# Kernel tuning notes

Hardware: AMD Instinct MI355X
Metric: run time of the kernel (lower is better)

## Reference

```python
import jax, jax.numpy as jnp
import numpy as np

M, K, N = 65536, 512, 512
EPS = 1e-05


def setup_inputs() -> dict:
    key = jax.random.key(0)
    k1, k2, k3 = jax.random.split(key, 3)
    x = jax.random.normal(k1, (M, K), dtype=jnp.float32)
    # int8 weight buffer in [-128, 127]
    weight_int8 = jax.random.randint(k2, (N, K), -128, 128, dtype=jnp.int32).astype(jnp.int8)
    # realistic per-output-channel dequant scales (max-abs / 127 of an fp weight)
    weight_scale = jax.random.uniform(k3, (N,), dtype=jnp.float32, minval=0.001, maxval=0.02)
    return {"x": x, "weight_int8": weight_int8, "weight_scale": weight_scale}


def reference(x, weight_int8, weight_scale):
    # dynamic per-tensor quantization of the activation
    x_scale = jnp.maximum(jnp.max(jnp.abs(x)) / 127.0, EPS)
    x_int8 = jnp.clip(jnp.round(x / x_scale), -128, 127).astype(jnp.int8)
    out_int32 = jnp.matmul(x_int8, weight_int8.T, preferred_element_type=jnp.int32)
    # dequantize: per-tensor input scale * per-row weight scale
    out = out_int32.astype(jnp.float32) * (x_scale * weight_scale[None, :])
    return out
```

## Files before the change

### kernel.cpp

```cpp
#include <hip/hip_runtime.h>


#define M_DIM 65536
#define K_DIM 512
#define N_DIM 512
#define EPSF  1e-5f

typedef int int32x4 __attribute__((ext_vector_type(4)));

#define WS_PART   256
#define WS_WPACK  32768

__device__ inline unsigned int pack_w4(int4 v) {
    return (v.x & 0xff) | ((v.y & 0xff) << 8) |
           ((v.z & 0xff) << 16) | ((unsigned)v.w << 24);
}

__device__ inline unsigned int quantpack4(float4 f, float inv) {
    const float C = 12582912.0f;
    unsigned int u0 = __float_as_uint(fmaf(f.x, inv, C));
    unsigned int u1 = __float_as_uint(fmaf(f.y, inv, C));
    unsigned int u2 = __float_as_uint(fmaf(f.z, inv, C));
    unsigned int u3 = __float_as_uint(fmaf(f.w, inv, C));
    unsigned int lo = __builtin_amdgcn_perm(u1, u0, 0x0C0C0400u);
    unsigned int hi = __builtin_amdgcn_perm(u3, u2, 0x04000C0Cu);
    return lo | hi;
}

__global__ void absmax1_pack_kernel(const float* __restrict__ x,
                                    const int* __restrict__ wi,
                                    float* __restrict__ partials,
                                    unsigned int* __restrict__ wp) {
    const int b = blockIdx.x;
    const int t = threadIdx.x;
    if (b < 4096) {
        __shared__ float red[4];
        const float4* x4 = (const float4*)x;
        const int base = b * 2048;
        float m = 0.0f;
        #pragma unroll
        for (int j = 0; j < 8; ++j) {
            float4 v = x4[base + j * 256 + t];
            m = fmaxf(m, fmaxf(fmaxf(fabsf(v.x), fabsf(v.y)),
                               fmaxf(fabsf(v.z), fabsf(v.w))));
        }
        #pragma unroll
        for (int off = 32; off > 0; off >>= 1)
            m = fmaxf(m, __shfl_xor(m, off));
        if ((t & 63) == 0) red[t >> 6] = m;
        __syncthreads();
        if (t == 0)
            partials[b] = fmaxf(fmaxf(red[0], red[1]), fmaxf(red[2], red[3]));
    } else {
        const int bb = b - 4096;
        #pragma unroll
        for (int j = 0; j < 4; ++j) {
            int d = bb * 1024 + j * 256 + t;
            wp[d] = pack_w4(((const int4*)wi)[d]);
        }
    }
}

__global__ __launch_bounds__(256, 2) void fused_quant_gemm_kernel(
    const float* __restrict__ x, const signed char* __restrict__ w,
    const float* __restrict__ wscale, const float* __restrict__ partials,
    float* __restrict__ out) {
    __shared__ __attribute__((aligned(16))) signed char Lds[64 * 1024];
    __shared__ float red[4];

    const int t    = threadIdx.x;
    const int wave = t >> 6;
    const int lane = t & 63;
    const int quad = lane >> 4;
    const int l16  = lane & 15;
    const int m0   = blockIdx.x * 128;

    float m = 0.0f;
    {
        const float4* p4 = (const float4*)partials;
        #pragma unroll
        for (int j = 0; j < 4; ++j) {
            float4 v = p4[t + j * 256];
            m = fmaxf(m, fmaxf(fmaxf(v.x, v.y), fmaxf(v.z, v.w)));
        }
        #pragma unroll
        for (int off = 32; off > 0; off >>= 1)
            m = fmaxf(m, __shfl_xor(m, off));
        if (lane == 0) red[wave] = m;
    }
    __syncthreads();
    const float mx  = fmaxf(fmaxf(red[0], red[1]), fmaxf(red[2], red[3]));
    const float s   = fmaxf(mx / 127.0f, EPSF);
    const float inv = 1.0f / s;
    __syncthreads();

    {
        const float4* xs = (const float4*)(x + (size_t)m0 * K_DIM);
        const int rsub = t >> 5;
        const int csub = (t & 31) * 16;
        #pragma unroll
        for (int j = 0; j < 16; ++j) {
            const int fi = j * 1024 + t * 4;
            float4 v0 = xs[fi + 0];
            float4 v1 = xs[fi + 1];
            float4 v2 = xs[fi + 2];
            float4 v3 = xs[fi + 3];
            int32x4 p;
            p.x = (int)quantpack4(v0, inv);
            p.y = (int)quantpack4(v1, inv);
            p.z = (int)quantpack4(v2, inv);
            p.w = (int)quantpack4(v3, inv);
            const int row  = j * 8 + rsub;
            const int addr = (row * 512 + csub) ^ ((row & 7) << 4);
            *(int32x4*)(Lds + addr) = p;
        }
    }
    __syncthreads();

    int32x4 a0[8], a1[8];
    {
        const int r0 = wave * 32 + l16;
        const int r1 = r0 + 16;
        #pragma unroll
        for (int k = 0; k < 8; ++k) {
            const int c = quad * 16 + k * 64;
            a0[k] = *(const int32x4*)(Lds + ((r0 * 512 + c) ^ ((r0 & 7) << 4)));
            a1[k] = *(const int32x4*)(Lds + ((r1 * 512 + c) ^ ((r1 & 7) << 4)));
        }
    }
    __syncthreads();

    const int mw = m0 + wave * 32;

    for (int bx = 0; bx < 4; ++bx) {
        const int n0 = bx * 128;

        #pragma unroll
        for (int cc = 0; cc < 2; ++cc) {
            int c = wave * 2 + cc;
            #pragma unroll
            for (int tt = 0; tt < 8; ++tt) {
                const signed char* g = w + (long)(n0 + tt * 16 + l16) * K_DIM
                                         + c * 64 + quad * 16;
                __builtin_amdgcn_global_load_lds(
                    (const __attribute__((address_space(1))) unsigned int*)g,
                    (__attribute__((address_space(3))) unsigned int*)(Lds + (c * 8 + tt) * 1024),
                    16, 0, 0);
            }
        }
        __syncthreads();

        int32x4 acc0[8] = {};
        int32x4 acc1[8] = {};
        #pragma unroll
        for (int k = 0; k < 8; ++k) {
            const signed char* bbase = Lds + k * 8192 + lane * 16;
            #pragma unroll
            for (int tt = 0; tt < 8; ++tt) {
                int32x4 b = *(const int32x4*)(bbase + tt * 1024);
                acc0[tt] = __builtin_amdgcn_mfma_i32_16x16x64_i8(a0[k], b, acc0[tt], 0, 0, 0);
                acc1[tt] = __builtin_amdgcn_mfma_i32_16x16x64_i8(a1[k], b, acc1[tt], 0, 0, 0);
            }
        }

        #pragma unroll
        for (int tt = 0; tt < 8; ++tt) {
            int n = n0 + tt * 16 + l16;
            float c = s * wscale[n];
            float* o0 = out + (long)(mw + quad * 4) * N_DIM + n;
            float* o1 = o0 + (long)16 * N_DIM;
            #pragma unroll
            for (int r = 0; r < 4; ++r) {
                o0[(long)r * N_DIM] = (float)acc0[tt][r] * c;
                o1[(long)r * N_DIM] = (float)acc1[tt][r] * c;
            }
        }
        if (bx < 3) __syncthreads();
    }
}

extern "C" void kernel_launch(void* const* d_in, const int* in_sizes, int n_in,
                              void* d_out, int out_size, void* d_ws, size_t ws_size,
                              hipStream_t stream) {
    const float* x   = (const float*)d_in[0];
    const int*   wi  = (const int*)d_in[1];
    const float* sc  = (const float*)d_in[2];
    float*       out = (float*)d_out;

    float*        partials = (float*)((char*)d_ws + WS_PART);
    unsigned int* wp       = (unsigned int*)((char*)d_ws + WS_WPACK);
    const signed char* w8  = (const signed char*)wp;

    absmax1_pack_kernel<<<4160, 256, 0, stream>>>(x, wi, partials, wp);
    fused_quant_gemm_kernel<<<512, 256, 0, stream>>>(x, w8, sc, partials, out);
}
```

Measured before the change: 265.7 us.

## Fuse absmax and GEMM into one persistent kernel with grid-wide atomic barrier

Merges the absmax/weight-pack kernel into the GEMM kernel. Each block computes its own tile's absmax while holding half of its activations in registers, then joins a grid-wide barrier built on an atomic counter before quantizing directly into MFMA A fragments, which skips the LDS staging round trip. The weight tile load for the next N-block is now issued before the current block's output stores, so the fetch overlaps the epilogue. The barrier relies on all 512 blocks being co-resident, and the large register array (h[32] plus the fragments) raises register pressure, which risks spills or deadlock if occupancy assumptions fail.

After: 381.2 us. 43.5% more time.

```diff
diff --git a/kernel.cpp b/kernel.cpp
--- a/kernel.cpp
+++ b/kernel.cpp
@@ -5,9 +5,11 @@
 #define K_DIM 512
 #define N_DIM 512
 #define EPSF  1e-5f
+#define GRID  512
 
 typedef int int32x4 __attribute__((ext_vector_type(4)));
 
+#define WS_CNT    0
 #define WS_PART   256
 #define WS_WPACK  32768
 
@@ -27,139 +29,162 @@
     return lo | hi;
 }
 
-__global__ void absmax1_pack_kernel(const float* __restrict__ x,
-                                    const int* __restrict__ wi,
-                                    float* __restrict__ partials,
-                                    unsigned int* __restrict__ wp) {
-    const int b = blockIdx.x;
-    const int t = threadIdx.x;
-    if (b < 4096) {
-        __shared__ float red[4];
-        const float4* x4 = (const float4*)x;
-        const int base = b * 2048;
-        float m = 0.0f;
-        #pragma unroll
-        for (int j = 0; j < 8; ++j) {
-            float4 v = x4[base + j * 256 + t];
-            m = fmaxf(m, fmaxf(fmaxf(fabsf(v.x), fabsf(v.y)),
-                               fmaxf(fabsf(v.z), fabsf(v.w))));
-        }
-        #pragma unroll
-        for (int off = 32; off > 0; off >>= 1)
-            m = fmaxf(m, __shfl_xor(m, off));
-        if ((t & 63) == 0) red[t >> 6] = m;
-        __syncthreads();
-        if (t == 0)
-            partials[b] = fmaxf(fmaxf(red[0], red[1]), fmaxf(red[2], red[3]));
-    } else {
-        const int bb = b - 4096;
-        #pragma unroll
-        for (int j = 0; j < 4; ++j) {
-            int d = bb * 1024 + j * 256 + t;
-            wp[d] = pack_w4(((const int4*)wi)[d]);
-        }
-    }
-}
-
-__global__ __launch_bounds__(256, 2) void fused_quant_gemm_kernel(
-    const float* __restrict__ x, const signed char* __restrict__ w,
-    const float* __restrict__ wscale, const float* __restrict__ partials,
+__global__ __launch_bounds__(256, 2) void fused_kernel(
+    const float* __restrict__ x, const int* __restrict__ wi,
+    const float* __restrict__ wscale, unsigned int* __restrict__ ws,
     float* __restrict__ out) {
-    __shared__ __attribute__((aligned(16))) signed char Lds[64 * 1024];
+    __shared__ __attribute__((aligned(16))) signed char Blds[64 * 1024];
     __shared__ float red[4];
+
+    unsigned int* cnt      = ws + (WS_CNT >> 2);
+    unsigned int* partials = ws + (WS_PART >> 2);
+    unsigned int* wp       = ws + (WS_WPACK >> 2);
+    const signed char* w8  = (const signed char*)wp;
 
     const int t    = threadIdx.x;
     const int wave = t >> 6;
     const int lane = t & 63;
     const int quad = lane >> 4;
     const int l16  = lane & 15;
-    const int m0   = blockIdx.x * 128;
-
+    const int b    = blockIdx.x;
+    const int m0   = b * 128;
+    const int mw   = m0 + wave * 32;
+
+    const float* xr0 = x + (size_t)(mw + l16) * K_DIM + quad * 16;
+    const float* xr1 = xr0 + (size_t)16 * K_DIM;
+
+    float4 h[32];
     float m = 0.0f;
+    #pragma unroll
+    for (int k = 0; k < 8; ++k) {
+        #pragma unroll
+        for (int j = 0; j < 4; ++j) {
+            float4 v = *(const float4*)(xr0 + k * 64 + j * 4);
+            h[k * 4 + j] = v;
+            m = fmaxf(m, fmaxf(fmaxf(fabsf(v.x), fabsf(v.y)),
+                               fmaxf(fabsf(v.z), fabsf(v.w))));
+        }
+    }
+    #pragma unroll
+    for (int k = 0; k < 8; ++k) {
+        #pragma unroll
+        for (int j = 0; j < 4; ++j) {
+            float4 v = *(const float4*)(xr1 + k * 64 + j * 4);
+            m = fmaxf(m, fmaxf(fmaxf(fabsf(v.x), fabsf(v.y)),
+                               fmaxf(fabsf(v.z), fabsf(v.w))));
+        }
+    }
+
+    if (b < 64) {
+        #pragma unroll
+        for (int j = 0; j < 4; ++j) {
+            int d = b * 1024 + j * 256 + t;
+            wp[d] = pack_w4(((const int4*)wi)[d]);
+        }
+    }
+
+    #pragma unroll
+    for (int off = 32; off > 0; off >>= 1)
+        m = fmaxf(m, __shfl_xor(m, off));
+    if (lane == 0) red[wave] = m;
+    __syncthreads();
+    if (t == 0)
+        partials[b] = __float_as_uint(
+            fmaxf(fmaxf(red[0], red[1]), fmaxf(red[2], red[3])));
+
+    __threadfence();
+    __syncthreads();
+    if (t == 0) {
+        __hip_atomic_fetch_add(cnt, 1u, __ATOMIC_ACQ_REL,
+                               __HIP_MEMORY_SCOPE_AGENT);
+        while (__hip_atomic_load(cnt, __ATOMIC_ACQUIRE,
+                                 __HIP_MEMORY_SCOPE_AGENT) != GRID)
+            __builtin_amdgcn_s_sleep(8);
+    }
+    __syncthreads();
+
+    #pragma unroll
+    for (int cc = 0; cc < 2; ++cc) {
+        int c = wave * 2 + cc;
+        #pragma unroll
+        for (int tt = 0; tt < 8; ++tt) {
+            const signed char* g = w8 + (long)(tt * 16 + l16) * K_DIM
+                                      + c * 64 + quad * 16;
+            __builtin_amdgcn_global_load_lds(
+                (const __attribute__((address_space(1))) unsigned int*)g,
+                (__attribute__((address_space(3))) unsigned int*)(Blds + (c * 8 + tt) * 1024),
+                16, 0, 0);
+        }
+    }
+
     {
-        const float4* p4 = (const float4*)partials;
-        #pragma unroll
-        for (int j = 0; j < 4; ++j) {
-            float4 v = p4[t + j * 256];
-            m = fmaxf(m, fmaxf(fmaxf(v.x, v.y), fmaxf(v.z, v.w)));
-        }
+        float v0 = __uint_as_float(__hip_atomic_load(
+            &partials[t], __ATOMIC_RELAXED, __HIP_MEMORY_SCOPE_AGENT));
+        float v1 = __uint_as_float(__hip_atomic_load(
+            &partials[t + 256], __ATOMIC_RELAXED, __HIP_MEMORY_SCOPE_AGENT));
+        float mm = fmaxf(v0, v1);
         #pragma unroll
         for (int off = 32; off > 0; off >>= 1)
-            m = fmaxf(m, __shfl_xor(m, off));
-        if (lane == 0) red[wave] = m;
+            mm = fmaxf(mm, __shfl_xor(mm, off));
+        if (lane == 0) red[wave] = mm;
     }
     __syncthreads();
     const float mx  = fmaxf(fmaxf(red[0], red[1]), fmaxf(red[2], red[3]));
     const float s   = fmaxf(mx / 127.0f, EPSF);
     const float inv = 1.0f / s;
-    __syncthreads();
-
-    {
-        const float4* xs = (const float4*)(x + (size_t)m0 * K_DIM);
-        const int rsub = t >> 5;
-        const int csub = (t & 31) * 16;
-        #pragma unroll
-        for (int j = 0; j < 16; ++j) {
-            const int fi = j * 1024 + t * 4;
-            float4 v0 = xs[fi + 0];
-            float4 v1 = xs[fi + 1];
-            float4 v2 = xs[fi + 2];
-            float4 v3 = xs[fi + 3];
-            int32x4 p;
-            p.x = (int)quantpack4(v0, inv);
-            p.y = (int)quantpack4(v1, inv);
-            p.z = (int)quantpack4(v2, inv);
-            p.w = (int)quantpack4(v3, inv);
-            const int row  = j * 8 + rsub;
-            const int addr = (row * 512 + csub) ^ ((row & 7) << 4);
-            *(int32x4*)(Lds + addr) = p;
-        }
-    }
-    __syncthreads();
 
     int32x4 a0[8], a1[8];
-    {
-        const int r0 = wave * 32 + l16;
-        const int r1 = r0 + 16;
-        #pragma unroll
-        for (int k = 0; k < 8; ++k) {
-            const int c = quad * 16 + k * 64;
-            a0[k] = *(const int32x4*)(Lds + ((r0 * 512 + c) ^ ((r0 & 7) << 4)));
-            a1[k] = *(const int32x4*)(Lds + ((r1 * 512 + c) ^ ((r1 & 7) << 4)));
-        }
-    }
-    __syncthreads();
-
-    const int mw = m0 + wave * 32;
+    #pragma unroll
+    for (int k = 0; k < 8; ++k) {
+        a0[k].x = (int)quantpack4(h[k * 4 + 0], inv);
+        a0[k].y = (int)quantpack4(h[k * 4 + 1], inv);
+        a0[k].z = (int)quantpack4(h[k * 4 + 2], inv);
+        a0[k].w = (int)quantpack4(h[k * 4 + 3], inv);
+    }
+    #pragma unroll
+    for (int k = 0; k < 8; ++k) {
+        float4 v0 = *(const float4*)(xr1 + k * 64 + 0);
+        float4 v1 = *(const float4*)(xr1 + k * 64 + 4);
+        float4 v2 = *(const float4*)(xr1 + k * 64 + 8);
+        float4 v3 = *(const float4*)(xr1 + k * 64 + 12);
+        a1[k].x = (int)quantpack4(v0, inv);
+        a1[k].y = (int)quantpack4(v1, inv);
+        a1[k].z = (int)quantpack4(v2, inv);
+        a1[k].w = (int)quantpack4(v3, inv);
+    }
 
     for (int bx = 0; bx < 4; ++bx) {
         const int n0 = bx * 128;
-
-        #pragma unroll
-        for (int cc = 0; cc < 2; ++cc) {
-            int c = wave * 2 + cc;
+        __syncthreads();
+
+        int32x4 acc0[8] = {};
+        int32x4 acc1[8] = {};
+        #pragma unroll
+        for (int k = 0; k < 8; ++k) {
+            const signed char* bbase = Blds + k * 8192 + lane * 16;
             #pragma unroll
             for (int tt = 0; tt < 8; ++tt) {
-                const signed char* g = w + (long)(n0 + tt * 16 + l16) * K_DIM
-                                         + c * 64 + quad * 16;
-                __builtin_amdgcn_global_load_lds(
-                    (const __attribute__((address_space(1))) unsigned int*)g,
-                    (__attribute__((address_space(3))) unsigned int*)(Lds + (c * 8 + tt) * 1024),
-                    16, 0, 0);
+                int32x4 bfrag = *(const int32x4*)(bbase + tt * 1024);
+                acc0[tt] = __builtin_amdgcn_mfma_i32_16x16x64_i8(a0[k], bfrag, acc0[tt], 0, 0, 0);
+                acc1[tt] = __builtin_amdgcn_mfma_i32_16x16x64_i8(a1[k], bfrag, acc1[tt], 0, 0, 0);
             }
         }
         __syncthreads();
 
-        int32x4 acc0[8] = {};
-        int32x4 acc1[8] = {};
-        #pragma unroll
-        for (int k = 0; k < 8; ++k) {
-            const signed char* bbase = Lds + k * 8192 + lane * 16;
+        if (bx < 3) {
+            const int n1 = (bx + 1) * 128;
             #pragma unroll
-            for (int tt = 0; tt < 8; ++tt) {
-                int32x4 b = *(const int32x4*)(bbase + tt * 1024);
-                acc0[tt] = __builtin_amdgcn_mfma_i32_16x16x64_i8(a0[k], b, acc0[tt], 0, 0, 0);
-                acc1[tt] = __builtin_amdgcn_mfma_i32_16x16x64_i8(a1[k], b, acc1[tt], 0, 0, 0);
+            for (int cc = 0; cc < 2; ++cc) {
+                int c = wave * 2 + cc;
+                #pragma unroll
+                for (int tt = 0; tt < 8; ++tt) {
+                    const signed char* g = w8 + (long)(n1 + tt * 16 + l16) * K_DIM
+                                              + c * 64 + quad * 16;
+                    __builtin_amdgcn_global_load_lds(
+                        (const __attribute__((address_space(1))) unsigned int*)g,
+                        (__attribute__((address_space(3))) unsigned int*)(Blds + (c * 8 + tt) * 1024),
+                        16, 0, 0);
+                }
             }
         }
 
@@ -175,7 +200,6 @@
                 o1[(long)r * N_DIM] = (float)acc1[tt][r] * c;
             }
         }
-        if (bx < 3) __syncthreads();
     }
 }
 
@@ -187,10 +211,7 @@
     const float* sc  = (const float*)d_in[2];
     float*       out = (float*)d_out;
 
-    float*        partials = (float*)((char*)d_ws + WS_PART);
-    unsigned int* wp       = (unsigned int*)((char*)d_ws + WS_WPACK);
-    const signed char* w8  = (const signed char*)wp;
-
-    absmax1_pack_kernel<<<4160, 256, 0, stream>>>(x, wi, partials, wp);
-    fused_quant_gemm_kernel<<<512, 256, 0, stream>>>(x, w8, sc, partials, out);
-}
+    hipMemsetAsync(d_ws, 0, 4, stream);
+
+    fused_kernel<<<GRID, 256, 0, stream>>>(x, wi, sc, (unsigned int*)d_ws, out);
+}
```

## Shrink GEMM tile to 64 rows, load A directly to registers, overlap B prefetch

Applied to the files above, without the earlier changes.

The GEMM block now covers 64 rows instead of 128 and 64-column weight chunks instead of 128, which halves LDS to 32 KB and raises the occupancy target to 4 blocks per CU across 1024 blocks. Activations are loaded from global memory, quantized, and packed straight into MFMA A-fragment registers, skipping the LDS staging and swizzle. The first weight chunk is issued before the absmax reduction, and each following chunk is issued right after the MFMAs and before the output stores, so weight loads overlap the epilogue. In exchange, each block loads its weight data as 8 chunks instead of 4, and the A-fragment global loads are less coalesced (16-float segments per lane).

New measurement: 279.9 us. +5.3%, slower.

```diff
diff --git a/kernel.cpp b/kernel.cpp
--- a/kernel.cpp
+++ b/kernel.cpp
@@ -61,11 +61,11 @@
     }
 }
 
-__global__ __launch_bounds__(256, 2) void fused_quant_gemm_kernel(
+__global__ __launch_bounds__(256, 4) void quant_gemm_kernel(
     const float* __restrict__ x, const signed char* __restrict__ w,
     const float* __restrict__ wscale, const float* __restrict__ partials,
     float* __restrict__ out) {
-    __shared__ __attribute__((aligned(16))) signed char Lds[64 * 1024];
+    __shared__ __attribute__((aligned(16))) signed char Blds[32 * 1024];
     __shared__ float red[4];
 
     const int t    = threadIdx.x;
@@ -73,7 +73,22 @@
     const int lane = t & 63;
     const int quad = lane >> 4;
     const int l16  = lane & 15;
-    const int m0   = blockIdx.x * 128;
+    const int m0   = blockIdx.x * 64;
+    const int mw   = m0 + wave * 16;
+
+    #pragma unroll
+    for (int cc = 0; cc < 2; ++cc) {
+        int c = wave * 2 + cc;
+        #pragma unroll
+        for (int tt = 0; tt < 4; ++tt) {
+            const signed char* g = w + (long)(tt * 16 + l16) * K_DIM
+                                     + c * 64 + quad * 16;
+            __builtin_amdgcn_global_load_lds(
+                (const __attribute__((address_space(1))) unsigned int*)g,
+                (__attribute__((address_space(3))) unsigned int*)(Blds + (c * 4 + tt) * 1024),
+                16, 0, 0);
+        }
+    }
 
     float m = 0.0f;
     {
@@ -92,90 +107,65 @@
     const float mx  = fmaxf(fmaxf(red[0], red[1]), fmaxf(red[2], red[3]));
     const float s   = fmaxf(mx / 127.0f, EPSF);
     const float inv = 1.0f / s;
-    __syncthreads();
 
+    int32x4 a[8];
     {
-        const float4* xs = (const float4*)(x + (size_t)m0 * K_DIM);
-        const int rsub = t >> 5;
-        const int csub = (t & 31) * 16;
+        const float* xr = x + (size_t)(mw + l16) * K_DIM + quad * 16;
         #pragma unroll
-        for (int j = 0; j < 16; ++j) {
-            const int fi = j * 1024 + t * 4;
-            float4 v0 = xs[fi + 0];
-            float4 v1 = xs[fi + 1];
-            float4 v2 = xs[fi + 2];
-            float4 v3 = xs[fi + 3];
-            int32x4 p;
-            p.x = (int)quantpack4(v0, inv);
-            p.y = (int)quantpack4(v1, inv);
-            p.z = (int)quantpack4(v2, inv);
-            p.w = (int)quantpack4(v3, inv);
-            const int row  = j * 8 + rsub;
-            const int addr = (row * 512 + csub) ^ ((row & 7) << 4);
-            *(int32x4*)(Lds + addr) = p;
+        for (int k = 0; k < 8; ++k) {
+            float4 v0 = *(const float4*)(xr + k * 64 + 0);
+            float4 v1 = *(const float4*)(xr + k * 64 + 4);
+            float4 v2 = *(const float4*)(xr + k * 64 + 8);
+            float4 v3 = *(const float4*)(xr + k * 64 + 12);
+            a[k].x = (int)quantpack4(v0, inv);
+            a[k].y = (int)quantpack4(v1, inv);
+            a[k].z = (int)quantpack4(v2, inv);
+            a[k].w = (int)quantpack4(v3, inv);
         }
     }
-    __syncthreads();
 
-    int32x4 a0[8], a1[8];
-    {
-        const int r0 = wave * 32 + l16;
-        const int r1 = r0 + 16;
+    for (int bx = 0; bx < 8; ++bx) {
+        const int n0 = bx * 64;
+        __syncthreads();
+
+        int32x4 acc[4] = {};
         #pragma unroll
         for (int k = 0; k < 8; ++k) {
-            const int c = quad * 16 + k * 64;
-            a0[k] = *(const int32x4*)(Lds + ((r0 * 512 + c) ^ ((r0 & 7) << 4)));
-            a1[k] = *(const int32x4*)(Lds + ((r1 * 512 + c) ^ ((r1 & 7) << 4)));
-        }
-    }
-    __syncthreads();
-
-    const int mw = m0 + wave * 32;
-
-    for (int bx = 0; bx < 4; ++bx) {
-        const int n0 = bx * 128;
-
-        #pragma unroll
-        for (int cc = 0; cc < 2; ++cc) {
-            int c = wave * 2 + cc;
+            const signed char* bbase = Blds + k * 4096 + lane * 16;
             #pragma unroll
-            for (int tt = 0; tt < 8; ++tt) {
-                const signed char* g = w + (long)(n0 + tt * 16 + l16) * K_DIM
-                                         + c * 64 + quad * 16;
-                __builtin_amdgcn_global_load_lds(
-                    (const __attribute__((address_space(1))) unsigned int*)g,
-                    (__attribute__((address_space(3))) unsigned int*)(Lds + (c * 8 + tt) * 1024),
-                    16, 0, 0);
+            for (int tt = 0; tt < 4; ++tt) {
+                int32x4 bf = *(const int32x4*)(bbase + tt * 1024);
+                acc[tt] = __builtin_amdgcn_mfma_i32_16x16x64_i8(a[k], bf, acc[tt], 0, 0, 0);
             }
         }
         __syncthreads();
 
-        int32x4 acc0[8] = {};
-        int32x4 acc1[8] = {};
-        #pragma unroll
-        for (int k = 0; k < 8; ++k) {
-            const signed char* bbase = Lds + k * 8192 + lane * 16;
+        if (bx < 7) {
+            const int n1 = (bx + 1) * 64;
             #pragma unroll
-            for (int tt = 0; tt < 8; ++tt) {
-                int32x4 b = *(const int32x4*)(bbase + tt * 1024);
-                acc0[tt] = __builtin_amdgcn_mfma_i32_16x16x64_i8(a0[k], b, acc0[tt], 0, 0, 0);
-                acc1[tt] = __builtin_amdgcn_mfma_i32_16x16x64_i8(a1[k], b, acc1[tt], 0, 0, 0);
+            for (int cc = 0; cc < 2; ++cc) {
+                int c = wave * 2 + cc;
+                #pragma unroll
+                for (int tt = 0; tt < 4; ++tt) {
+                    const signed char* g = w + (long)(n1 + tt * 16 + l16) * K_DIM
+                                             + c * 64 + quad * 16;
+                    __builtin_amdgcn_global_load_lds(
+                        (const __attribute__((address_space(1))) unsigned int*)g,
+                        (__attribute__((address_space(3))) unsigned int*)(Blds + (c * 4 + tt) * 1024),
+                        16, 0, 0);
+                }
             }
         }
 
         #pragma unroll
-        for (int tt = 0; tt < 8; ++tt) {
+        for (int tt = 0; tt < 4; ++tt) {
             int n = n0 + tt * 16 + l16;
             float c = s * wscale[n];
-            float* o0 = out + (long)(mw + quad * 4) * N_DIM + n;
-            float* o1 = o0 + (long)16 * N_DIM;
+            float* o = out + (long)(mw + quad * 4) * N_DIM + n;
             #pragma unroll
-            for (int r = 0; r < 4; ++r) {
-                o0[(long)r * N_DIM] = (float)acc0[tt][r] * c;
-                o1[(long)r * N_DIM] = (float)acc1[tt][r] * c;
-            }
+            for (int r = 0; r < 4; ++r)
+                o[(long)r * N_DIM] = (float)acc[tt][r] * c;
         }
-        if (bx < 3) __syncthreads();
     }
 }
 
@@ -192,5 +182,5 @@
     const signed char* w8  = (const signed char*)wp;
 
     absmax1_pack_kernel<<<4160, 256, 0, stream>>>(x, wi, partials, wp);
-    fused_quant_gemm_kernel<<<512, 256, 0, stream>>>(x, w8, sc, partials, out);
+    quant_gemm_kernel<<<1024, 256, 0, stream>>>(x, w8, sc, partials, out);
 }
```

## Use atomic absmax, prefetch next weight tile before epilogue, stagger N order

Applied to the files above, without the earlier changes.

Replaces the per-block partials array with a single atomicMax on the float bits, which removes the partial-reduction prologue and two barriers from the GEMM kernel but adds a memset launch and 4096 contending atomics. The next weight tile's global-to-LDS load is now issued before the epilogue stores, so the weight fetch overlaps the output writes. Blocks also start at different N tiles to spread accesses to the weight rows. The float-as-uint atomicMax is valid only because the values are non-negative.

After: 273.5 us. 2.9% more time.

```diff
diff --git a/kernel.cpp b/kernel.cpp
--- a/kernel.cpp
+++ b/kernel.cpp
@@ -8,7 +8,7 @@
 
 typedef int int32x4 __attribute__((ext_vector_type(4)));
 
-#define WS_PART   256
+#define WS_ABS    0
 #define WS_WPACK  32768
 
 __device__ inline unsigned int pack_w4(int4 v) {
@@ -29,7 +29,7 @@
 
 __global__ void absmax1_pack_kernel(const float* __restrict__ x,
                                     const int* __restrict__ wi,
-                                    float* __restrict__ partials,
+                                    unsigned int* __restrict__ ws_abs,
                                     unsigned int* __restrict__ wp) {
     const int b = blockIdx.x;
     const int t = threadIdx.x;
@@ -49,8 +49,10 @@
             m = fmaxf(m, __shfl_xor(m, off));
         if ((t & 63) == 0) red[t >> 6] = m;
         __syncthreads();
-        if (t == 0)
-            partials[b] = fmaxf(fmaxf(red[0], red[1]), fmaxf(red[2], red[3]));
+        if (t == 0) {
+            float bm = fmaxf(fmaxf(red[0], red[1]), fmaxf(red[2], red[3]));
+            atomicMax(ws_abs, __float_as_uint(bm));
+        }
     } else {
         const int bb = b - 4096;
         #pragma unroll
@@ -61,38 +63,23 @@
     }
 }
 
-__global__ __launch_bounds__(256, 2) void fused_quant_gemm_kernel(
+__global__ __launch_bounds__(256, 2) void quant_gemm_kernel(
     const float* __restrict__ x, const signed char* __restrict__ w,
-    const float* __restrict__ wscale, const float* __restrict__ partials,
+    const float* __restrict__ wscale, const unsigned int* __restrict__ ws_abs,
     float* __restrict__ out) {
     __shared__ __attribute__((aligned(16))) signed char Lds[64 * 1024];
-    __shared__ float red[4];
 
     const int t    = threadIdx.x;
     const int wave = t >> 6;
     const int lane = t & 63;
     const int quad = lane >> 4;
     const int l16  = lane & 15;
-    const int m0   = blockIdx.x * 128;
-
-    float m = 0.0f;
-    {
-        const float4* p4 = (const float4*)partials;
-        #pragma unroll
-        for (int j = 0; j < 4; ++j) {
-            float4 v = p4[t + j * 256];
-            m = fmaxf(m, fmaxf(fmaxf(v.x, v.y), fmaxf(v.z, v.w)));
-        }
-        #pragma unroll
-        for (int off = 32; off > 0; off >>= 1)
-            m = fmaxf(m, __shfl_xor(m, off));
-        if (lane == 0) red[wave] = m;
-    }
-    __syncthreads();
-    const float mx  = fmaxf(fmaxf(red[0], red[1]), fmaxf(red[2], red[3]));
+    const int b    = blockIdx.x;
+    const int m0   = b * 128;
+
+    const float mx  = __uint_as_float(ws_abs[0]);
     const float s   = fmaxf(mx / 127.0f, EPSF);
     const float inv = 1.0f / s;
-    __syncthreads();
 
     {
         const float4* xs = (const float4*)(x + (size_t)m0 * K_DIM);
@@ -132,9 +119,10 @@
 
     const int mw = m0 + wave * 32;
 
-    for (int bx = 0; bx < 4; ++bx) {
-        const int n0 = bx * 128;
-
+    const int start = ((b ^ (b >> 8)) & 1) * 2;
+
+    {
+        const int n0 = ((start) & 3) * 128;
         #pragma unroll
         for (int cc = 0; cc < 2; ++cc) {
             int c = wave * 2 + cc;
@@ -148,6 +136,11 @@
                     16, 0, 0);
             }
         }
+    }
+
+    for (int i = 0; i < 4; ++i) {
+        const int bx = (start + i) & 3;
+        const int n0 = bx * 128;
         __syncthreads();
 
         int32x4 acc0[8] = {};
@@ -157,9 +150,27 @@
             const signed char* bbase = Lds + k * 8192 + lane * 16;
             #pragma unroll
             for (int tt = 0; tt < 8; ++tt) {
-                int32x4 b = *(const int32x4*)(bbase + tt * 1024);
-                acc0[tt] = __builtin_amdgcn_mfma_i32_16x16x64_i8(a0[k], b, acc0[tt], 0, 0, 0);
-                acc1[tt] = __builtin_amdgcn_mfma_i32_16x16x64_i8(a1[k], b, acc1[tt], 0, 0, 0);
+                int32x4 bfrag = *(const int32x4*)(bbase + tt * 1024);
+                acc0[tt] = __builtin_amdgcn_mfma_i32_16x16x64_i8(a0[k], bfrag, acc0[tt], 0, 0, 0);
+                acc1[tt] = __builtin_amdgcn_mfma_i32_16x16x64_i8(a1[k], bfrag, acc1[tt], 0, 0, 0);
+            }
+        }
+        __syncthreads();
+
+        if (i < 3) {
+            const int n1 = ((start + i + 1) & 3) * 128;
+            #pragma unroll
+            for (int cc = 0; cc < 2; ++cc) {
+                int c = wave * 2 + cc;
+                #pragma unroll
+                for (int tt = 0; tt < 8; ++tt) {
+                    const signed char* g = w + (long)(n1 + tt * 16 + l16) * K_DIM
+                                             + c * 64 + quad * 16;
+                    __builtin_amdgcn_global_load_lds(
+                        (const __attribute__((address_space(1))) unsigned int*)g,
+                        (__attribute__((address_space(3))) unsigned int*)(Lds + (c * 8 + tt) * 1024),
+                        16, 0, 0);
+                }
             }
         }
 
@@ -175,7 +186,6 @@
                 o1[(long)r * N_DIM] = (float)acc1[tt][r] * c;
             }
         }
-        if (bx < 3) __syncthreads();
     }
 }
 
@@ -187,10 +197,12 @@
     const float* sc  = (const float*)d_in[2];
     float*       out = (float*)d_out;
 
-    float*        partials = (float*)((char*)d_ws + WS_PART);
-    unsigned int* wp       = (unsigned int*)((char*)d_ws + WS_WPACK);
-    const signed char* w8  = (const signed char*)wp;
-
-    absmax1_pack_kernel<<<4160, 256, 0, stream>>>(x, wi, partials, wp);
-    fused_quant_gemm_kernel<<<512, 256, 0, stream>>>(x, w8, sc, partials, out);
-}
+    unsigned int* ws_abs = (unsigned int*)d_ws;
+    unsigned int* wp     = (unsigned int*)((char*)d_ws + WS_WPACK);
+    const signed char* w8 = (const signed char*)wp;
+
+    hipMemsetAsync(d_ws, 0, 4, stream);
+
+    absmax1_pack_kernel<<<4160, 256, 0, stream>>>(x, wi, ws_abs, wp);
+    quant_gemm_kernel<<<512, 256, 0, stream>>>(x, w8, sc, ws_abs, out);
+}
```
